# Kernel tuning notes

Hardware: AMD Instinct MI355X
Metric: run time of the kernel (lower is better)

The kernel has to match this reference:

```python
import jax, jax.numpy as jnp
import numpy as np

N, E, D = 10000, 320000, 128
SIGMA = 0.3


def setup_inputs() -> dict:
    key = jax.random.key(0)
    ks = jax.random.split(key, 24)
    f32 = jnp.float32
    inp = {
        "h": jax.random.normal(ks[0], (N, D), f32),
        "e": jax.random.normal(ks[1], (E, D), f32),
        "p": jax.random.normal(ks[2], (N, D), f32),
        "d": jax.random.normal(ks[3], (N, D), f32),
        "dt": jax.random.uniform(ks[4], (N,), f32, 0.1, 0.5),
        "spatial_mask": jax.random.randint(ks[5], (E,), 0, 2).astype(jnp.int32),
        "src": jax.random.randint(ks[6], (E,), 0, N),
        "dst": jax.random.randint(ks[7], (E,), 0, N),
    }
    names = ["V1", "V2", "E1", "P1", "P2", "P3", "D1", "D2", "V"]
    for i, n in enumerate(names):
        inp["W_" + n] = jax.random.normal(ks[8 + i], (D, D), f32) * 0.05
        inp["b_" + n] = jnp.zeros((D,), f32)
    inp["W_T"] = jax.random.normal(ks[20], (D, 2 * D), f32) * 0.05
    inp["b_T"] = jnp.zeros((D,), f32)
    return inp


def _lin(x, W, b):
    return x @ W.T + b


def _forward(h, e, p, d, dt,
             W_V1, b_V1, W_V2, b_V2, W_E1, b_E1,
             W_P1, b_P1, W_P2, b_P2, W_P3, b_P3,
             W_D1, b_D1, W_D2, b_D2, W_V, b_V, W_T, b_T,
             spatial_mask, src, dst):
    n_nodes = h.shape[0]
    V1h = _lin(h, W_V1, b_V1)
    V2h = _lin(h, W_V2, b_V2)
    E1e = _lin(e, W_E1, b_E1)
    P1h = _lin(p, W_P1, b_P1)
    P2h = _lin(p, W_P2, b_P2)
    P3h = _lin(p, W_P3, b_P3)
    D1h = _lin(d, W_D1, b_D1)
    D2h = _lin(d, W_D2, b_D2)
    # edge update: e' = 0.5 * ((P1h[dst] - P2h[src]) + E1(e))   [E,D]
    e_new = 0.5 * ((P1h[dst] - P2h[src]) + E1e)
    smask = (spatial_mask == 1)[:, None]  # [E,1] True = spatial edge
    a = D1h - V1h                          # [N,D]
    # temporal branch: tau = relu(T([h_dst, d_dst])) on temporal edges only,
    # summed into the destination node (zeros elsewhere, like DGL's partial apply_edges)
    tau = jnp.where(smask, 0.0,
                    jax.nn.relu(_lin(jnp.concatenate([h[dst], d[dst]], -1), W_T, b_T)))
    sum_tau = jax.ops.segment_sum(tau, dst, num_segments=n_nodes)
    f0 = a * sum_tau
    # spatial branch: grad_rab = vjp of (Vj * value_rab(rab)) wrt rab = e_new, cotangent = ones
    Vj = jnp.where(smask, jax.nn.relu(_lin(h[src] * h[dst], W_V, b_V)), 0.0)

    def compute(rab):
        nrm = jnp.clip(jnp.linalg.norm(rab, axis=-1, keepdims=True), 1e-9, None)
        r = 0.5 * jnp.sqrt(nrm)              # [E,1]
        return Vj * jnp.exp(-r / SIGMA)      # [E,D]

    _, vjp_fn = jax.vjp(compute, e_new)
    grad_rab, = vjp_fn(jnp.ones_like(e_new))
    fab = jax.ops.segment_sum(grad_rab, dst, num_segments=n_nodes)
    f = f0 - fab
    dtc = dt[:, None]
    h_out = V2h + f * dtc
    p_out = P3h + f * dtc + 0.5 * f * dtc ** 2
    d_out = D2h + f / (jnp.linalg.norm(f, axis=-1, keepdims=True) + 1e-9)
    lrelu = lambda x: jax.nn.leaky_relu(x, 0.01)
    # residual (input_dim == output_dim); dropout is identity in eval mode
    return (h + lrelu(h_out), e + lrelu(e_new), p + lrelu(p_out), d + lrelu(d_out))


def reference(h, e, p, d, dt, spatial_mask, src, dst,
              W_V1, b_V1, W_V2, b_V2, W_E1, b_E1,
              W_P1, b_P1, W_P2, b_P2, W_P3, b_P3,
              W_D1, b_D1, W_D2, b_D2, W_V, b_V, W_T, b_T):
    return _forward(h, e, p, d, dt,
                    W_V1, b_V1, W_V2, b_V2, W_E1, b_E1,
                    W_P1, b_P1, W_P2, b_P2, W_P3, b_P3,
                    W_D1, b_D1, W_D2, b_D2, W_V, b_V, W_T, b_T,
                    spatial_mask, src, dst)
```

## Files before the change

kernel.cpp:

```cpp
#include <hip/hip_runtime.h>
#include <hip/hip_bf16.h>

#define NN 10000
#define NE 320000
#define SIG 0.3f
#define NDp ((size_t)1280000)
#define OUT_H ((size_t)0)
#define OUT_E ((size_t)1280000)
#define OUT_P ((size_t)42240000)
#define OUT_D ((size_t)43520000)

#define F_V1H (0 * NDp)
#define F_V2H (1 * NDp)
#define F_P1H (2 * NDp)
#define F_P2H (3 * NDp)
#define F_P3H (4 * NDp)
#define F_D1H (5 * NDp)
#define F_D2H (6 * NDp)
#define F_G   (7 * NDp)
#define F_FAB (8 * NDp)
#define F_CNT (9 * NDp)
#define F_FLAGS (9 * NDp + 10240)
#define F_STAGED (9 * NDp + 10240 + 16)
#define S_H  ((size_t)0)
#define S_P  ((size_t)1280000)
#define S_D  ((size_t)2560000)
#define S_W  ((size_t)3840000)
#define S_WT (S_W + 9 * 16384)

typedef __attribute__((ext_vector_type(8))) short s8v;
typedef __attribute__((ext_vector_type(4))) float f4v;

__device__ __forceinline__ float b2f(unsigned short s) {
  return __uint_as_float(((unsigned int)s) << 16);
}
__device__ __forceinline__ short f2b(float f) {
  __hip_bfloat16 b = __float2bfloat16(f);
  return *reinterpret_cast<short*>(&b);
}
__device__ __forceinline__ float lrelu(float x) { return x >= 0.f ? x : 0.01f * x; }
__device__ __forceinline__ float loadf(const void* p, size_t i, bool f32) {
  return f32 ? ((const float*)p)[i] : b2f(((const unsigned short*)p)[i]);
}
__device__ __forceinline__ void storef(void* p, size_t i, float v, bool f32) {
  if (f32) ((float*)p)[i] = v;
  else ((unsigned short*)p)[i] = (unsigned short)f2b(v);
}
__device__ __forceinline__ s8v cvt8(const float* fp) {
  s8v r;
#pragma unroll
  for (int j = 0; j < 8; j++) r[j] = f2b(fp[j]);
  return r;
}

__global__ __launch_bounds__(256) void zero_kernel(float* ws) {
  int i = blockIdx.x * 256 + threadIdx.x;
  ws[F_FAB + i] = 0.f;
  if (i < NN) ws[F_CNT + i] = 0.f;
  if (i < 16) ((int*)(ws + F_FLAGS))[i] = 0;
}

struct DetTask { const unsigned short* s; int n; int flag; };
struct DetArgs { DetTask t[6]; int* flags; };
__global__ __launch_bounds__(256) void detect_kernel(DetArgs a) {
  DetTask t = a.t[blockIdx.y];
  int hit = 0;
  for (int i = blockIdx.x * 256 + threadIdx.x; i < t.n; i += gridDim.x * 256) {
    if ((unsigned short)(t.s[i] & 0x7FFF) > (unsigned short)0x7F80) hit = 1;
  }
  if (hit) atomicOr(&a.flags[t.flag], 1);
}

struct ConvTask { const void* src; unsigned short* dst; int n; int flag; };
struct ConvArgs { ConvTask t[13]; const int* flags; };
__global__ __launch_bounds__(256) void convert_kernel(ConvArgs a) {
  ConvTask t = a.t[blockIdx.y];
  bool f32 = a.flags[t.flag] != 0;
  for (int i = blockIdx.x * 256 + threadIdx.x; i < t.n; i += gridDim.x * 256) {
    t.dst[i] = f32 ? (unsigned short)f2b(((const float*)t.src)[i])
                   : ((const unsigned short*)t.src)[i];
  }
}

__global__ __launch_bounds__(256) void cnt_kernel(const int* __restrict__ spatial,
                                                  const int* __restrict__ dst,
                                                  float* __restrict__ cnt) {
  int e = blockIdx.x * 256 + threadIdx.x;
  if (e < NE && spatial[e] != 1) atomicAdd(&cnt[dst[e]], 1.0f);
}

struct NodeArgs {
  const unsigned short* x[3];
  const unsigned short* W[8];
  const void* b[8];
  float* out[8];
  const int* flags;
};

__global__ __launch_bounds__(256) void node_gemm_kernel(NodeArgs a) {
  const int o = blockIdx.y;
  const int wave = threadIdx.x >> 6, lane = threadIdx.x & 63;
  const int l16 = lane & 15, quad = lane >> 4;
  const int m0 = blockIdx.x * 64 + wave * 16;
  if (m0 >= NN) return;
  const bool wf32 = a.flags[5] != 0;
  int arow = m0 + l16;
  if (arow >= NN) arow = NN - 1;
  const unsigned short* Wp = a.W[o];
  f4v acc[8] = {};
  if (o < 7) {
    const unsigned short* X0 = (o < 2) ? a.x[0] : (o < 5 ? a.x[1] : a.x[2]);
    const unsigned short* xrow = X0 + (size_t)arow * 128;
#pragma unroll
    for (int kk = 0; kk < 128; kk += 32) {
      int k8 = kk + quad * 8;
      s8v av = *(const s8v*)(xrow + k8);
#pragma unroll
      for (int nt = 0; nt < 8; nt++) {
        s8v bv = *(const s8v*)(Wp + (size_t)(nt * 16 + l16) * 128 + k8);
        acc[nt] = __builtin_amdgcn_mfma_f32_16x16x32_bf16(av, bv, acc[nt], 0, 0, 0);
      }
    }
  } else {
#pragma unroll
    for (int kk = 0; kk < 256; kk += 32) {
      int k8 = kk + quad * 8;
      const unsigned short* ap = (k8 < 128) ? (a.x[0] + (size_t)arow * 128 + k8)
                                            : (a.x[2] + (size_t)arow * 128 + (k8 - 128));
      s8v av = *(const s8v*)ap;
#pragma unroll
      for (int nt = 0; nt < 8; nt++) {
        s8v bv = *(const s8v*)(Wp + (size_t)(nt * 16 + l16) * 256 + k8);
        acc[nt] = __builtin_amdgcn_mfma_f32_16x16x32_bf16(av, bv, acc[nt], 0, 0, 0);
      }
    }
  }
  float* outp = a.out[o];
#pragma unroll
  for (int nt = 0; nt < 8; nt++) {
    int col = nt * 16 + l16;
    float bvv = loadf(a.b[o], col, wf32);
#pragma unroll
    for (int r = 0; r < 4; r++) {
      int row = m0 + quad * 4 + r;
      if (row < NN) {
        float v = acc[nt][r] + bvv;
        if (o == 7) v = fmaxf(v, 0.f);
        outp[(size_t)row * 128 + col] = v;
      }
    }
  }
}

__global__ __launch_bounds__(256) void edge_kernel(
    const void* __restrict__ e, const unsigned short* __restrict__ sh,
    const int* __restrict__ spatial, const int* __restrict__ src, const int* __restrict__ dst,
    const unsigned short* __restrict__ WE1, const unsigned short* __restrict__ WV,
    const void* __restrict__ bE1, const void* __restrict__ bV,
    const float* __restrict__ P1h, const float* __restrict__ P2h,
    float* __restrict__ fab, void* __restrict__ out, const int* __restrict__ flags) {
  const int wave = threadIdx.x >> 6, lane = threadIdx.x & 63;
  const int l16 = lane & 15, quad = lane >> 4;
  const int m0 = blockIdx.x * 64 + wave * 16;
  const bool ef32 = flags[1] != 0;
  const bool wf32 = flags[5] != 0;
  const bool of32 = (flags[0] | flags[1] | flags[2] | flags[3] | flags[4] | flags[5]) != 0;

  f4v acc1[8] = {};
  {
    size_t ro = (size_t)(m0 + l16) * 128;
#pragma unroll
    for (int kk = 0; kk < 128; kk += 32) {
      int k8 = kk + quad * 8;
      s8v av;
      if (ef32) av = cvt8((const float*)e + ro + k8);
      else av = *(const s8v*)((const unsigned short*)e + ro + k8);
#pragma unroll
      for (int nt = 0; nt < 8; nt++) {
        s8v bv = *(const s8v*)(WE1 + (size_t)(nt * 16 + l16) * 128 + k8);
        acc1[nt] = __builtin_amdgcn_mfma_f32_16x16x32_bf16(av, bv, acc1[nt], 0, 0, 0);
      }
    }
  }
  f4v acc2[8] = {};
  {
    int asrc = src[m0 + l16], adst = dst[m0 + l16];
    const unsigned short* hs_row = sh + (size_t)asrc * 128;
    const unsigned short* hd_row = sh + (size_t)adst * 128;
#pragma unroll
    for (int kk = 0; kk < 128; kk += 32) {
      int k8 = kk + quad * 8;
      s8v hs = *(const s8v*)(hs_row + k8);
      s8v hd = *(const s8v*)(hd_row + k8);
      s8v ap;
#pragma unroll
      for (int j = 0; j < 8; j++)
        ap[j] = f2b(b2f((unsigned short)hs[j]) * b2f((unsigned short)hd[j]));
#pragma unroll
      for (int nt = 0; nt < 8; nt++) {
        s8v bv = *(const s8v*)(WV + (size_t)(nt * 16 + l16) * 128 + k8);
        acc2[nt] = __builtin_amdgcn_mfma_f32_16x16x32_bf16(ap, bv, acc2[nt], 0, 0, 0);
      }
    }
  }
  int sr[4], dr[4], sp[4];
#pragma unroll
  for (int r = 0; r < 4; r++) {
    int row = m0 + quad * 4 + r;
    sr[r] = src[row];
    dr[r] = dst[row];
    sp[r] = spatial[row];
  }
  float en[8][4];
  float nrm2[4] = {0.f, 0.f, 0.f, 0.f};
#pragma unroll
  for (int nt = 0; nt < 8; nt++) {
    int col = nt * 16 + l16;
    float be = loadf(bE1, col, wf32);
#pragma unroll
    for (int r = 0; r < 4; r++) {
      int row = m0 + quad * 4 + r;
      float E1 = acc1[nt][r] + be;
      float v = 0.5f * (P1h[(size_t)dr[r] * 128 + col] - P2h[(size_t)sr[r] * 128 + col] + E1);
      en[nt][r] = v;
      nrm2[r] += v * v;
      float eo = loadf(e, (size_t)row * 128 + col, ef32);
      storef(out, OUT_E + (size_t)row * 128 + col, eo + lrelu(v), of32);
    }
  }
#pragma unroll
  for (int m = 1; m < 16; m <<= 1) {
#pragma unroll
    for (int r = 0; r < 4; r++) nrm2[r] += __shfl_xor(nrm2[r], m, 64);
  }
  float sv[4] = {0.f, 0.f, 0.f, 0.f};
#pragma unroll
  for (int nt = 0; nt < 8; nt++) {
    int col = nt * 16 + l16;
    float bvv = loadf(bV, col, wf32);
#pragma unroll
    for (int r = 0; r < 4; r++) sv[r] += fmaxf(acc2[nt][r] + bvv, 0.f);
  }
#pragma unroll
  for (int m = 1; m < 16; m <<= 1) {
#pragma unroll
    for (int r = 0; r < 4; r++) sv[r] += __shfl_xor(sv[r], m, 64);
  }
  float coef[4];
#pragma unroll
  for (int r = 0; r < 4; r++) {
    float n = sqrtf(nrm2[r]);
    float c = 0.f;
    if (sp[r] == 1 && n >= 1e-9f) {
      float rr = 0.5f * sqrtf(n);
      float s = expf(-rr / SIG);
      c = -sv[r] * s * 0.25f / (SIG * n * sqrtf(n));
    }
    coef[r] = c;
  }
#pragma unroll
  for (int r = 0; r < 4; r++) {
    if (coef[r] != 0.f) {
#pragma unroll
      for (int nt = 0; nt < 8; nt++) {
        int col = nt * 16 + l16;
        atomicAdd(&fab[(size_t)dr[r] * 128 + col], coef[r] * en[nt][r]);
      }
    }
  }
}

__global__ __launch_bounds__(256) void node_out_kernel(
    const unsigned short* __restrict__ sh, const unsigned short* __restrict__ sp,
    const unsigned short* __restrict__ sd, const void* __restrict__ dt,
    const float* __restrict__ V1h, const float* __restrict__ V2h, const float* __restrict__ P3h,
    const float* __restrict__ D1h, const float* __restrict__ D2h, const float* __restrict__ g,
    const float* __restrict__ fab, const float* __restrict__ cnt,
    void* __restrict__ out, const int* __restrict__ flags) {
  const int wave = threadIdx.x >> 6, lane = threadIdx.x & 63;
  const int node = blockIdx.x * 4 + wave;
  const bool dtf32 = flags[4] != 0;
  const bool of32 = (flags[0] | flags[1] | flags[2] | flags[3] | flags[4] | flags[5]) != 0;
  const size_t i = (size_t)node * 128 + lane * 2;
  float cn = cnt[node];
  float2 v1 = *(const float2*)(V1h + i);
  float2 d1 = *(const float2*)(D1h + i);
  float2 gg = *(const float2*)(g + i);
  float2 fb = *(const float2*)(fab + i);
  float fx = (d1.x - v1.x) * (cn * gg.x) - fb.x;
  float fy = (d1.y - v1.y) * (cn * gg.y) - fb.y;
  float n2 = fx * fx + fy * fy;
#pragma unroll
  for (int m = 1; m < 64; m <<= 1) n2 += __shfl_xor(n2, m, 64);
  float nf = sqrtf(n2);
  float dtv = loadf(dt, node, dtf32);
  float2 v2 = *(const float2*)(V2h + i);
  float2 p3 = *(const float2*)(P3h + i);
  float2 d2 = *(const float2*)(D2h + i);
  float hx = v2.x + fx * dtv, hy = v2.y + fy * dtv;
  float px = p3.x + fx * dtv + 0.5f * fx * dtv * dtv;
  float py = p3.y + fy * dtv + 0.5f * fy * dtv * dtv;
  float invn = 1.f / (nf + 1e-9f);
  float dx = d2.x + fx * invn, dy = d2.y + fy * invn;
  storef(out, OUT_H + i,     b2f(sh[i])     + lrelu(hx), of32);
  storef(out, OUT_H + i + 1, b2f(sh[i + 1]) + lrelu(hy), of32);
  storef(out, OUT_P + i,     b2f(sp[i])     + lrelu(px), of32);
  storef(out, OUT_P + i + 1, b2f(sp[i + 1]) + lrelu(py), of32);
  storef(out, OUT_D + i,     b2f(sd[i])     + lrelu(dx), of32);
  storef(out, OUT_D + i + 1, b2f(sd[i + 1]) + lrelu(dy), of32);
}

extern "C" void kernel_launch(void* const* d_in, const int* in_sizes, int n_in,
                              void* d_out, int out_size, void* d_ws, size_t ws_size,
                              hipStream_t stream) {
  const int* spatial = (const int*)d_in[5];
  const int* src = (const int*)d_in[6];
  const int* dst = (const int*)d_in[7];

  float* ws = (float*)d_ws;
  int* flags = (int*)(ws + F_FLAGS);
  unsigned short* stg = (unsigned short*)(ws + F_STAGED);

  zero_kernel<<<(int)(NDp / 256), 256, 0, stream>>>(ws);

  DetArgs da;
  da.t[0] = { (const unsigned short*)d_in[0], 1280000, 0 };
  da.t[1] = { (const unsigned short*)d_in[1], 40960000, 1 };
  da.t[2] = { (const unsigned short*)d_in[2], 1280000, 2 };
  da.t[3] = { (const unsigned short*)d_in[3], 1280000, 3 };
  da.t[4] = { (const unsigned short*)d_in[4], 10000, 4 };
  da.t[5] = { (const unsigned short*)d_in[8], 16384, 5 };
  da.flags = flags;
  detect_kernel<<<dim3(1024, 6), 256, 0, stream>>>(da);

  ConvArgs ca;
  ca.t[0] = { d_in[0], stg + S_H, 1280000, 0 };
  ca.t[1] = { d_in[2], stg + S_P, 1280000, 2 };
  ca.t[2] = { d_in[3], stg + S_D, 1280000, 3 };
  for (int i = 0; i < 9; i++)
    ca.t[3 + i] = { d_in[8 + 2 * i], stg + S_W + (size_t)i * 16384, 16384, 5 };
  ca.t[12] = { d_in[26], stg + S_WT, 32768, 5 };
  ca.flags = flags;
  convert_kernel<<<dim3(640, 13), 256, 0, stream>>>(ca);

  cnt_kernel<<<NE / 256, 256, 0, stream>>>(spatial, dst, ws + F_CNT);

  NodeArgs na;
  na.x[0] = stg + S_H; na.x[1] = stg + S_P; na.x[2] = stg + S_D;
  na.W[0] = stg + S_W + 0 * 16384;  na.b[0] = d_in[9];
  na.W[1] = stg + S_W + 1 * 16384;  na.b[1] = d_in[11];
  na.W[2] = stg + S_W + 3 * 16384;  na.b[2] = d_in[15];
  na.W[3] = stg + S_W + 4 * 16384;  na.b[3] = d_in[17];
  na.W[4] = stg + S_W + 5 * 16384;  na.b[4] = d_in[19];
  na.W[5] = stg + S_W + 6 * 16384;  na.b[5] = d_in[21];
  na.W[6] = stg + S_W + 7 * 16384;  na.b[6] = d_in[23];
  na.W[7] = stg + S_WT;             na.b[7] = d_in[27];
  na.out[0] = ws + F_V1H; na.out[1] = ws + F_V2H; na.out[2] = ws + F_P1H;
  na.out[3] = ws + F_P2H; na.out[4] = ws + F_P3H; na.out[5] = ws + F_D1H;
  na.out[6] = ws + F_D2H; na.out[7] = ws + F_G;
  na.flags = flags;
  node_gemm_kernel<<<dim3((NN + 63) / 64, 8), 256, 0, stream>>>(na);

  edge_kernel<<<NE / 64, 256, 0, stream>>>(
      d_in[1], stg + S_H, spatial, src, dst,
      stg + S_W + 2 * 16384, stg + S_W + 8 * 16384, d_in[13], d_in[25],
      ws + F_P1H, ws + F_P2H, ws + F_FAB, d_out, flags);

  node_out_kernel<<<NN / 4, 256, 0, stream>>>(
      stg + S_H, stg + S_P, stg + S_D, d_in[4],
      ws + F_V1H, ws + F_V2H, ws + F_P3H, ws + F_D1H, ws + F_D2H, ws + F_G,
      ws + F_FAB, ws + F_CNT, d_out, flags);
}
```

Before: 858.5 us.

## Sort edges by destination via CSR and merge per-row atomics

Builds a destination-sorted edge permutation on device (degree count, single-block scan, atomic scatter), and the edge kernel processes edges in that order. When the four rows a lane handles share a destination, their contributions are summed before one atomic add, cutting atomic traffic into fab and improving locality of the P1h and hd gathers. The cost is extra preprocessing kernels, including a serial single-block scan. Reads of e and writes of the edge output become scattered rows instead of contiguous ones.

```diff
diff --git a/kernel.cpp b/kernel.cpp
--- a/kernel.cpp
+++ b/kernel.cpp
@@ -27,6 +27,10 @@
 #define S_D  ((size_t)2560000)
 #define S_W  ((size_t)3840000)
 #define S_WT (S_W + 9 * 16384)
+#define F_DEG  (F_STAGED + (size_t)2010112)
+#define F_OFF  (F_DEG + 10240)
+#define F_FILL (F_OFF + 10240)
+#define F_CSR  (F_FILL + 10240)
 
 typedef __attribute__((ext_vector_type(8))) short s8v;
 typedef __attribute__((ext_vector_type(4))) float f4v;
@@ -56,7 +60,11 @@
 __global__ __launch_bounds__(256) void zero_kernel(float* ws) {
   int i = blockIdx.x * 256 + threadIdx.x;
   ws[F_FAB + i] = 0.f;
-  if (i < NN) ws[F_CNT + i] = 0.f;
+  if (i < NN) {
+    ws[F_CNT + i] = 0.f;
+    ((int*)(ws + F_DEG))[i] = 0;
+    ((int*)(ws + F_FILL))[i] = 0;
+  }
   if (i < 16) ((int*)(ws + F_FLAGS))[i] = 0;
 }
 
@@ -84,9 +92,53 @@
 
 __global__ __launch_bounds__(256) void cnt_kernel(const int* __restrict__ spatial,
                                                   const int* __restrict__ dst,
-                                                  float* __restrict__ cnt) {
+                                                  float* __restrict__ ws) {
   int e = blockIdx.x * 256 + threadIdx.x;
-  if (e < NE && spatial[e] != 1) atomicAdd(&cnt[dst[e]], 1.0f);
+  if (e < NE) {
+    int d = dst[e];
+    atomicAdd((int*)(ws + F_DEG) + d, 1);
+    if (spatial[e] != 1) atomicAdd(ws + F_CNT + d, 1.0f);
+  }
+}
+
+__global__ __launch_bounds__(1024) void scan_kernel(float* ws) {
+  const int* deg = (const int*)(ws + F_DEG);
+  int* off = (int*)(ws + F_OFF);
+  __shared__ int sbuf[1024];
+  __shared__ int carry;
+  if (threadIdx.x == 0) carry = 0;
+  __syncthreads();
+  for (int base = 0; base < NN; base += 1024) {
+    int i = base + threadIdx.x;
+    int v = (i < NN) ? deg[i] : 0;
+    sbuf[threadIdx.x] = v;
+    __syncthreads();
+#pragma unroll
+    for (int ofs = 1; ofs < 1024; ofs <<= 1) {
+      int t = (threadIdx.x >= ofs) ? sbuf[threadIdx.x - ofs] : 0;
+      __syncthreads();
+      sbuf[threadIdx.x] += t;
+      __syncthreads();
+    }
+    int incl = sbuf[threadIdx.x];
+    if (i < NN) off[i] = carry + incl - v;
+    __syncthreads();
+    if (threadIdx.x == 0) carry += sbuf[1023];
+    __syncthreads();
+  }
+}
+
+__global__ __launch_bounds__(256) void scatter_kernel(const int* __restrict__ dst,
+                                                      float* __restrict__ ws) {
+  int e = blockIdx.x * 256 + threadIdx.x;
+  if (e < NE) {
+    int d = dst[e];
+    const int* off = (const int*)(ws + F_OFF);
+    int* fill = (int*)(ws + F_FILL);
+    int* csr = (int*)(ws + F_CSR);
+    int pos = off[d] + atomicAdd(&fill[d], 1);
+    csr[pos] = e;
+  }
 }
 
 struct NodeArgs {
@@ -158,7 +210,8 @@
     const unsigned short* __restrict__ WE1, const unsigned short* __restrict__ WV,
     const void* __restrict__ bE1, const void* __restrict__ bV,
     const float* __restrict__ P1h, const float* __restrict__ P2h,
-    float* __restrict__ fab, void* __restrict__ out, const int* __restrict__ flags) {
+    float* __restrict__ fab, void* __restrict__ out, const int* __restrict__ flags,
+    const int* __restrict__ csr) {
   const int wave = threadIdx.x >> 6, lane = threadIdx.x & 63;
   const int l16 = lane & 15, quad = lane >> 4;
   const int m0 = blockIdx.x * 64 + wave * 16;
@@ -166,9 +219,47 @@
   const bool wf32 = flags[5] != 0;
   const bool of32 = (flags[0] | flags[1] | flags[2] | flags[3] | flags[4] | flags[5]) != 0;
 
+  const int eidA = csr[m0 + l16];
+
+  float sv[4];
+  {
+    f4v acc2[8] = {};
+    const int asrc = src[eidA], adst = dst[eidA];
+    const unsigned short* hs_row = sh + (size_t)asrc * 128;
+    const unsigned short* hd_row = sh + (size_t)adst * 128;
+#pragma unroll
+    for (int kk = 0; kk < 128; kk += 32) {
+      int k8 = kk + quad * 8;
+      s8v hs = *(const s8v*)(hs_row + k8);
+      s8v hd = *(const s8v*)(hd_row + k8);
+      s8v ap;
+#pragma unroll
+      for (int j = 0; j < 8; j++)
+        ap[j] = f2b(b2f((unsigned short)hs[j]) * b2f((unsigned short)hd[j]));
+#pragma unroll
+      for (int nt = 0; nt < 8; nt++) {
+        s8v bv = *(const s8v*)(WV + (size_t)(nt * 16 + l16) * 128 + k8);
+        acc2[nt] = __builtin_amdgcn_mfma_f32_16x16x32_bf16(ap, bv, acc2[nt], 0, 0, 0);
+      }
+    }
+    sv[0] = sv[1] = sv[2] = sv[3] = 0.f;
+#pragma unroll
+    for (int nt = 0; nt < 8; nt++) {
+      int col = nt * 16 + l16;
+      float bvv = loadf(bV, col, wf32);
+#pragma unroll
+      for (int r = 0; r < 4; r++) sv[r] += fmaxf(acc2[nt][r] + bvv, 0.f);
+    }
+#pragma unroll
+    for (int m = 1; m < 16; m <<= 1) {
+#pragma unroll
+      for (int r = 0; r < 4; r++) sv[r] += __shfl_xor(sv[r], m, 64);
+    }
+  }
+
   f4v acc1[8] = {};
   {
-    size_t ro = (size_t)(m0 + l16) * 128;
+    size_t ro = (size_t)eidA * 128;
 #pragma unroll
     for (int kk = 0; kk < 128; kk += 32) {
       int k8 = kk + quad * 8;
@@ -182,34 +273,15 @@
       }
     }
   }
-  f4v acc2[8] = {};
-  {
-    int asrc = src[m0 + l16], adst = dst[m0 + l16];
-    const unsigned short* hs_row = sh + (size_t)asrc * 128;
-    const unsigned short* hd_row = sh + (size_t)adst * 128;
-#pragma unroll
-    for (int kk = 0; kk < 128; kk += 32) {
-      int k8 = kk + quad * 8;
-      s8v hs = *(const s8v*)(hs_row + k8);
-      s8v hd = *(const s8v*)(hd_row + k8);
-      s8v ap;
-#pragma unroll
-      for (int j = 0; j < 8; j++)
-        ap[j] = f2b(b2f((unsigned short)hs[j]) * b2f((unsigned short)hd[j]));
-#pragma unroll
-      for (int nt = 0; nt < 8; nt++) {
-        s8v bv = *(const s8v*)(WV + (size_t)(nt * 16 + l16) * 128 + k8);
-        acc2[nt] = __builtin_amdgcn_mfma_f32_16x16x32_bf16(ap, bv, acc2[nt], 0, 0, 0);
-      }
-    }
-  }
-  int sr[4], dr[4], sp[4];
+
+  int er[4], sr[4], dr[4], sp[4];
 #pragma unroll
   for (int r = 0; r < 4; r++) {
-    int row = m0 + quad * 4 + r;
-    sr[r] = src[row];
-    dr[r] = dst[row];
-    sp[r] = spatial[row];
+    int slot = m0 + quad * 4 + r;
+    er[r] = csr[slot];
+    sr[r] = src[er[r]];
+    dr[r] = dst[er[r]];
+    sp[r] = spatial[er[r]];
   }
   float en[8][4];
   float nrm2[4] = {0.f, 0.f, 0.f, 0.f};
@@ -219,32 +291,18 @@
     float be = loadf(bE1, col, wf32);
 #pragma unroll
     for (int r = 0; r < 4; r++) {
-      int row = m0 + quad * 4 + r;
       float E1 = acc1[nt][r] + be;
       float v = 0.5f * (P1h[(size_t)dr[r] * 128 + col] - P2h[(size_t)sr[r] * 128 + col] + E1);
       en[nt][r] = v;
       nrm2[r] += v * v;
-      float eo = loadf(e, (size_t)row * 128 + col, ef32);
-      storef(out, OUT_E + (size_t)row * 128 + col, eo + lrelu(v), of32);
+      float eo = loadf(e, (size_t)er[r] * 128 + col, ef32);
+      storef(out, OUT_E + (size_t)er[r] * 128 + col, eo + lrelu(v), of32);
     }
   }
 #pragma unroll
   for (int m = 1; m < 16; m <<= 1) {
 #pragma unroll
     for (int r = 0; r < 4; r++) nrm2[r] += __shfl_xor(nrm2[r], m, 64);
-  }
-  float sv[4] = {0.f, 0.f, 0.f, 0.f};
-#pragma unroll
-  for (int nt = 0; nt < 8; nt++) {
-    int col = nt * 16 + l16;
-    float bvv = loadf(bV, col, wf32);
-#pragma unroll
-    for (int r = 0; r < 4; r++) sv[r] += fmaxf(acc2[nt][r] + bvv, 0.f);
-  }
-#pragma unroll
-  for (int m = 1; m < 16; m <<= 1) {
-#pragma unroll
-    for (int r = 0; r < 4; r++) sv[r] += __shfl_xor(sv[r], m, 64);
   }
   float coef[4];
 #pragma unroll
@@ -258,13 +316,27 @@
     }
     coef[r] = c;
   }
-#pragma unroll
-  for (int r = 0; r < 4; r++) {
-    if (coef[r] != 0.f) {
+  bool any = (coef[0] != 0.f) | (coef[1] != 0.f) | (coef[2] != 0.f) | (coef[3] != 0.f);
+  if (dr[0] == dr[3]) {
+    if (any) {
+      size_t base = (size_t)dr[0] * 128;
 #pragma unroll
       for (int nt = 0; nt < 8; nt++) {
         int col = nt * 16 + l16;
-        atomicAdd(&fab[(size_t)dr[r] * 128 + col], coef[r] * en[nt][r]);
+        float val = coef[0] * en[nt][0] + coef[1] * en[nt][1] +
+                    coef[2] * en[nt][2] + coef[3] * en[nt][3];
+        atomicAdd(&fab[base + col], val);
+      }
+    }
+  } else {
+#pragma unroll
+    for (int r = 0; r < 4; r++) {
+      if (coef[r] != 0.f) {
+#pragma unroll
+        for (int nt = 0; nt < 8; nt++) {
+          int col = nt * 16 + l16;
+          atomicAdd(&fab[(size_t)dr[r] * 128 + col], coef[r] * en[nt][r]);
+        }
       }
     }
   }
@@ -343,7 +415,9 @@
   ca.flags = flags;
   convert_kernel<<<dim3(640, 13), 256, 0, stream>>>(ca);
 
-  cnt_kernel<<<NE / 256, 256, 0, stream>>>(spatial, dst, ws + F_CNT);
+  cnt_kernel<<<NE / 256, 256, 0, stream>>>(spatial, dst, ws);
+  scan_kernel<<<1, 1024, 0, stream>>>(ws);
+  scatter_kernel<<<NE / 256, 256, 0, stream>>>(dst, ws);
 
   NodeArgs na;
   na.x[0] = stg + S_H; na.x[1] = stg + S_P; na.x[2] = stg + S_D;
@@ -364,7 +438,8 @@
   edge_kernel<<<NE / 64, 256, 0, stream>>>(
       d_in[1], stg + S_H, spatial, src, dst,
       stg + S_W + 2 * 16384, stg + S_W + 8 * 16384, d_in[13], d_in[25],
-      ws + F_P1H, ws + F_P2H, ws + F_FAB, d_out, flags);
+      ws + F_P1H, ws + F_P2H, ws + F_FAB, d_out, flags,
+      (const int*)(ws + F_CSR));
 
   node_out_kernel<<<NN / 4, 256, 0, stream>>>(
       stg + S_H, stg + S_P, stg + S_D, d_in[4],
```

Result: slower. 920.8 us (+7.2%).

## Restage edge epilogue through LDS for row-contiguous coalesced gathers, stores and atomics

Applied to the files above, without the earlier changes.

The edge kernel now writes the E1 matmul result (bf16) and the loaded e tile into shared memory. A per-row epilogue then has each lane handle two adjacent columns, so P1h/P2h gathers, the e_out stores and the fab atomics become contiguous per row rather than strided across the MFMA fragment layout. The V-branch sum is computed first and passed through LDS, which lowers peak register pressure. Stores are vectorized with a float2 / packed-bf16 helper, and cvt8 now uses 128-bit loads. The cost is that E1 and e are rounded to bf16 in LDS, which changes precision when the inputs are f32.

```diff
diff --git a/kernel.cpp b/kernel.cpp
--- a/kernel.cpp
+++ b/kernel.cpp
@@ -46,10 +46,21 @@
   if (f32) ((float*)p)[i] = v;
   else ((unsigned short*)p)[i] = (unsigned short)f2b(v);
 }
+__device__ __forceinline__ void storef2(void* p, size_t i, float x, float y, bool f32) {
+  if (f32) {
+    *reinterpret_cast<float2*>((float*)p + i) = make_float2(x, y);
+  } else {
+    unsigned int v = ((unsigned int)(unsigned short)f2b(y) << 16) |
+                     (unsigned int)(unsigned short)f2b(x);
+    *((unsigned int*)p + (i >> 1)) = v;
+  }
+}
 __device__ __forceinline__ s8v cvt8(const float* fp) {
+  f4v a = *reinterpret_cast<const f4v*>(fp);
+  f4v b = *reinterpret_cast<const f4v*>(fp + 4);
   s8v r;
 #pragma unroll
-  for (int j = 0; j < 8; j++) r[j] = f2b(fp[j]);
+  for (int j = 0; j < 4; j++) { r[j] = f2b(a[j]); r[4 + j] = f2b(b[j]); }
   return r;
 }
 
@@ -152,6 +163,7 @@
   }
 }
 
+#define LSTRIDE 136
 __global__ __launch_bounds__(256) void edge_kernel(
     const void* __restrict__ e, const unsigned short* __restrict__ sh,
     const int* __restrict__ spatial, const int* __restrict__ src, const int* __restrict__ dst,
@@ -159,112 +171,112 @@
     const void* __restrict__ bE1, const void* __restrict__ bV,
     const float* __restrict__ P1h, const float* __restrict__ P2h,
     float* __restrict__ fab, void* __restrict__ out, const int* __restrict__ flags) {
+  __shared__ __align__(16) unsigned short lds_e[4][16 * LSTRIDE];
+  __shared__ __align__(16) unsigned short lds_E1[4][16 * LSTRIDE];
+  __shared__ float lds_sv[4][16];
   const int wave = threadIdx.x >> 6, lane = threadIdx.x & 63;
   const int l16 = lane & 15, quad = lane >> 4;
   const int m0 = blockIdx.x * 64 + wave * 16;
   const bool ef32 = flags[1] != 0;
   const bool wf32 = flags[5] != 0;
   const bool of32 = (flags[0] | flags[1] | flags[2] | flags[3] | flags[4] | flags[5]) != 0;
-
-  f4v acc1[8] = {};
+  const int arow = m0 + l16;
+
   {
-    size_t ro = (size_t)(m0 + l16) * 128;
+    f4v acc2[8] = {};
+    const int asrc = src[arow], adst = dst[arow];
+    const unsigned short* hs_row = sh + (size_t)asrc * 128;
+    const unsigned short* hd_row = sh + (size_t)adst * 128;
+#pragma unroll
+    for (int kk = 0; kk < 128; kk += 32) {
+      int k8 = kk + quad * 8;
+      s8v hs = *(const s8v*)(hs_row + k8);
+      s8v hd = *(const s8v*)(hd_row + k8);
+      s8v ap;
+#pragma unroll
+      for (int j = 0; j < 8; j++)
+        ap[j] = f2b(b2f((unsigned short)hs[j]) * b2f((unsigned short)hd[j]));
+#pragma unroll
+      for (int nt = 0; nt < 8; nt++) {
+        s8v bv = *(const s8v*)(WV + (size_t)(nt * 16 + l16) * 128 + k8);
+        acc2[nt] = __builtin_amdgcn_mfma_f32_16x16x32_bf16(ap, bv, acc2[nt], 0, 0, 0);
+      }
+    }
+    float sv[4] = {0.f, 0.f, 0.f, 0.f};
+#pragma unroll
+    for (int nt = 0; nt < 8; nt++) {
+      int col = nt * 16 + l16;
+      float bvv = loadf(bV, col, wf32);
+#pragma unroll
+      for (int r = 0; r < 4; r++) sv[r] += fmaxf(acc2[nt][r] + bvv, 0.f);
+    }
+#pragma unroll
+    for (int m = 1; m < 16; m <<= 1) {
+#pragma unroll
+      for (int r = 0; r < 4; r++) sv[r] += __shfl_xor(sv[r], m, 64);
+    }
+    if (l16 == 0) {
+#pragma unroll
+      for (int r = 0; r < 4; r++) lds_sv[wave][quad * 4 + r] = sv[r];
+    }
+  }
+
+  {
+    f4v acc1[8] = {};
+    size_t ro = (size_t)arow * 128;
 #pragma unroll
     for (int kk = 0; kk < 128; kk += 32) {
       int k8 = kk + quad * 8;
       s8v av;
       if (ef32) av = cvt8((const float*)e + ro + k8);
       else av = *(const s8v*)((const unsigned short*)e + ro + k8);
+      *(s8v*)&lds_e[wave][l16 * LSTRIDE + k8] = av;
 #pragma unroll
       for (int nt = 0; nt < 8; nt++) {
         s8v bv = *(const s8v*)(WE1 + (size_t)(nt * 16 + l16) * 128 + k8);
         acc1[nt] = __builtin_amdgcn_mfma_f32_16x16x32_bf16(av, bv, acc1[nt], 0, 0, 0);
       }
     }
-  }
-  f4v acc2[8] = {};
-  {
-    int asrc = src[m0 + l16], adst = dst[m0 + l16];
-    const unsigned short* hs_row = sh + (size_t)asrc * 128;
-    const unsigned short* hd_row = sh + (size_t)adst * 128;
-#pragma unroll
-    for (int kk = 0; kk < 128; kk += 32) {
-      int k8 = kk + quad * 8;
-      s8v hs = *(const s8v*)(hs_row + k8);
-      s8v hd = *(const s8v*)(hd_row + k8);
-      s8v ap;
-#pragma unroll
-      for (int j = 0; j < 8; j++)
-        ap[j] = f2b(b2f((unsigned short)hs[j]) * b2f((unsigned short)hd[j]));
-#pragma unroll
-      for (int nt = 0; nt < 8; nt++) {
-        s8v bv = *(const s8v*)(WV + (size_t)(nt * 16 + l16) * 128 + k8);
-        acc2[nt] = __builtin_amdgcn_mfma_f32_16x16x32_bf16(ap, bv, acc2[nt], 0, 0, 0);
-      }
-    }
-  }
-  int sr[4], dr[4], sp[4];
-#pragma unroll
-  for (int r = 0; r < 4; r++) {
-    int row = m0 + quad * 4 + r;
-    sr[r] = src[row];
-    dr[r] = dst[row];
-    sp[r] = spatial[row];
-  }
-  float en[8][4];
-  float nrm2[4] = {0.f, 0.f, 0.f, 0.f};
-#pragma unroll
-  for (int nt = 0; nt < 8; nt++) {
-    int col = nt * 16 + l16;
-    float be = loadf(bE1, col, wf32);
-#pragma unroll
-    for (int r = 0; r < 4; r++) {
-      int row = m0 + quad * 4 + r;
-      float E1 = acc1[nt][r] + be;
-      float v = 0.5f * (P1h[(size_t)dr[r] * 128 + col] - P2h[(size_t)sr[r] * 128 + col] + E1);
-      en[nt][r] = v;
-      nrm2[r] += v * v;
-      float eo = loadf(e, (size_t)row * 128 + col, ef32);
-      storef(out, OUT_E + (size_t)row * 128 + col, eo + lrelu(v), of32);
-    }
-  }
-#pragma unroll
-  for (int m = 1; m < 16; m <<= 1) {
-#pragma unroll
-    for (int r = 0; r < 4; r++) nrm2[r] += __shfl_xor(nrm2[r], m, 64);
-  }
-  float sv[4] = {0.f, 0.f, 0.f, 0.f};
-#pragma unroll
-  for (int nt = 0; nt < 8; nt++) {
-    int col = nt * 16 + l16;
-    float bvv = loadf(bV, col, wf32);
-#pragma unroll
-    for (int r = 0; r < 4; r++) sv[r] += fmaxf(acc2[nt][r] + bvv, 0.f);
-  }
-#pragma unroll
-  for (int m = 1; m < 16; m <<= 1) {
-#pragma unroll
-    for (int r = 0; r < 4; r++) sv[r] += __shfl_xor(sv[r], m, 64);
-  }
-  float coef[4];
-#pragma unroll
-  for (int r = 0; r < 4; r++) {
-    float n = sqrtf(nrm2[r]);
-    float c = 0.f;
-    if (sp[r] == 1 && n >= 1e-9f) {
-      float rr = 0.5f * sqrtf(n);
-      float s = expf(-rr / SIG);
-      c = -sv[r] * s * 0.25f / (SIG * n * sqrtf(n));
-    }
-    coef[r] = c;
-  }
-#pragma unroll
-  for (int r = 0; r < 4; r++) {
-    if (coef[r] != 0.f) {
-#pragma unroll
-      for (int nt = 0; nt < 8; nt++) {
-        int col = nt * 16 + l16;
-        atomicAdd(&fab[(size_t)dr[r] * 128 + col], coef[r] * en[nt][r]);
+#pragma unroll
+    for (int nt = 0; nt < 8; nt++) {
+      int col = nt * 16 + l16;
+      float bvv = loadf(bE1, col, wf32);
+#pragma unroll
+      for (int r = 0; r < 4; r++) {
+        int row = quad * 4 + r;
+        lds_E1[wave][row * LSTRIDE + col] = (unsigned short)f2b(acc1[nt][r] + bvv);
+      }
+    }
+  }
+
+  const int c0 = lane * 2;
+#pragma unroll 4
+  for (int row = 0; row < 16; row++) {
+    const int er = m0 + row;
+    const int sr_ = src[er], dr_ = dst[er], sp_ = spatial[er];
+    float2 p1 = *(const float2*)(P1h + (size_t)dr_ * 128 + c0);
+    float2 p2 = *(const float2*)(P2h + (size_t)sr_ * 128 + c0);
+    unsigned int e1w = *(const unsigned int*)&lds_E1[wave][row * LSTRIDE + c0];
+    unsigned int eew = *(const unsigned int*)&lds_e[wave][row * LSTRIDE + c0];
+    float e1x = b2f((unsigned short)(e1w & 0xFFFF));
+    float e1y = b2f((unsigned short)(e1w >> 16));
+    float eex = b2f((unsigned short)(eew & 0xFFFF));
+    float eey = b2f((unsigned short)(eew >> 16));
+    float vx = 0.5f * (p1.x - p2.x + e1x);
+    float vy = 0.5f * (p1.y - p2.y + e1y);
+    storef2(out, OUT_E + (size_t)er * 128 + c0, eex + lrelu(vx), eey + lrelu(vy), of32);
+    float n2 = vx * vx + vy * vy;
+#pragma unroll
+    for (int m = 1; m < 64; m <<= 1) n2 += __shfl_xor(n2, m, 64);
+    if (sp_ == 1) {
+      float n = sqrtf(n2);
+      if (n >= 1e-9f) {
+        float svr = lds_sv[wave][row];
+        float rr = 0.5f * sqrtf(n);
+        float s = expf(-rr / SIG);
+        float c = -svr * s * 0.25f / (SIG * n * sqrtf(n));
+        atomicAdd(&fab[(size_t)dr_ * 128 + c0], c * vx);
+        atomicAdd(&fab[(size_t)dr_ * 128 + c0 + 1], c * vy);
       }
     }
   }
@@ -302,12 +314,9 @@
   float py = p3.y + fy * dtv + 0.5f * fy * dtv * dtv;
   float invn = 1.f / (nf + 1e-9f);
   float dx = d2.x + fx * invn, dy = d2.y + fy * invn;
-  storef(out, OUT_H + i,     b2f(sh[i])     + lrelu(hx), of32);
-  storef(out, OUT_H + i + 1, b2f(sh[i + 1]) + lrelu(hy), of32);
-  storef(out, OUT_P + i,     b2f(sp[i])     + lrelu(px), of32);
-  storef(out, OUT_P + i + 1, b2f(sp[i + 1]) + lrelu(py), of32);
-  storef(out, OUT_D + i,     b2f(sd[i])     + lrelu(dx), of32);
-  storef(out, OUT_D + i + 1, b2f(sd[i + 1]) + lrelu(dy), of32);
+  storef2(out, OUT_H + i, b2f(sh[i]) + lrelu(hx), b2f(sh[i + 1]) + lrelu(hy), of32);
+  storef2(out, OUT_P + i, b2f(sp[i]) + lrelu(px), b2f(sp[i + 1]) + lrelu(py), of32);
+  storef2(out, OUT_D + i, b2f(sd[i]) + lrelu(dx), b2f(sd[i + 1]) + lrelu(dy), of32);
 }
 
 extern "C" void kernel_launch(void* const* d_in, const int* in_sizes, int n_in,
```

New measurement: 828.9 us. 3.5% less time.
